# Performance work log

Hardware: AMD Instinct MI355X
Metric: run time of the kernel (lower is better)

Reference implementation:

```python
import jax, jax.numpy as jnp
import numpy as np


def _unpack_int4(w_i32):
    # w_i32: [N, K//8] int32, 8 signed int4 nibbles per int32 (low nibble first)
    shifts = jnp.arange(8, dtype=jnp.int32) * 4
    nib = (w_i32[:, :, None] >> shifts[None, None, :]) & 0xF  # [N, K//8, 8]
    signed = (nib ^ 8) - 8  # map [0,15] -> [-8,7]
    N = w_i32.shape[0]
    return signed.reshape(N, -1)  # [N, K] int32 in [-8,7]


def setup_inputs() -> dict:
    key = jax.random.key(0)
    k1, k2, k3, k4, k5 = jax.random.split(key, 5)
    M, K, N, G = 4096, 4096, 14336, 128
    qx = jax.random.normal(k1, (M, K), dtype=jnp.float32)
    qxscale = jax.random.uniform(k2, (M, 1), dtype=jnp.float32, minval=0.5, maxval=1.5)
    weight_i4 = jax.random.randint(k3, (N, K // 8), 0, 2147483647, dtype=jnp.int32)
    weight_scale = jax.random.uniform(k4, (N, K // G), dtype=jnp.float32, minval=0.001, maxval=0.02)
    bias = jax.random.normal(k5, (N,), dtype=jnp.float32) * 0.02
    return {"qx": qx, "qxscale": qxscale, "weight_i4": weight_i4,
            "weight_scale": weight_scale, "bias": bias, "group_size": G}


def reference(qx, qxscale, weight_i4, weight_scale, bias, group_size):
    # 1) unpack int32 -> int4  2) per-group dequant  3) matmul  4) scale+bias  5) silu
    iweight = _unpack_int4(weight_i4)  # [N, K]
    N, K = iweight.shape
    deq_w = (iweight.astype(jnp.float32).reshape(N, K // group_size, group_size)
             * weight_scale[:, :, None]).reshape(N, K)  # [N, K]
    y = jnp.einsum('mk,nk->mn', qx, deq_w) * qxscale  # [M, N]
    y = y + bias[None, :]
    return jax.nn.silu(y)
```

## Files before the change

kernel.cpp:

```cpp
#include <hip/hip_runtime.h>
#include <hip/hip_bf16.h>
#include <stdint.h>


#define M_DIM 4096
#define K_DIM 4096
#define N_DIM 14336
#define GSZ   128

typedef __bf16 bf16x8 __attribute__((ext_vector_type(8)));
typedef __bf16 bf16x4 __attribute__((ext_vector_type(4)));
typedef float  f32x4  __attribute__((ext_vector_type(4)));

#define GLOAD16(g, l) __builtin_amdgcn_global_load_lds( \
    (const __attribute__((address_space(1))) void*)(g), \
    (__attribute__((address_space(3))) void*)(l), 16, 0, 0)

#define WAITVM(N) asm volatile("s_waitcnt vmcnt(" #N ")" ::: "memory")
#define WAITLGKM0() asm volatile("s_waitcnt lgkmcnt(0)" ::: "memory")


__global__ __launch_bounds__(256) void convertA_kernel(
    const float* __restrict__ qx, __bf16* __restrict__ out)
{
    const size_t i = ((size_t)blockIdx.x * 256 + threadIdx.x) * 8;
    const float4 a = *(const float4*)(qx + i);
    const float4 b = *(const float4*)(qx + i + 4);
    bf16x8 v;
    v[0] = (__bf16)a.x; v[1] = (__bf16)a.y; v[2] = (__bf16)a.z; v[3] = (__bf16)a.w;
    v[4] = (__bf16)b.x; v[5] = (__bf16)b.y; v[6] = (__bf16)b.z; v[7] = (__bf16)b.w;
    *(bf16x8*)(out + i) = v;
}

__global__ __launch_bounds__(256) void dequantW_kernel(
    const int* __restrict__ wq, const float* __restrict__ wscale,
    __bf16* __restrict__ out)
{
    const size_t g = (size_t)blockIdx.x * 256 + threadIdx.x;
    const int n  = (int)(g >> 9);
    const int wi = (int)(g & 511);
    const float s = wscale[(size_t)n * (K_DIM / GSZ) + (wi >> 4)];
    const int w = wq[g];
    bf16x8 v;
    #pragma unroll
    for (int j = 0; j < 8; ++j) {
        const int q = ((int)((unsigned)w << (28 - 4 * j))) >> 28;
        v[j] = (__bf16)((float)q * s);
    }
    *(bf16x8*)(out + g * 8) = v;
}


constexpr int BM = 256, BN = 256, BK = 64;
constexpr int NT  = K_DIM / BK;
constexpr int NIT = NT / 2;
constexpr int BUF_BYTES = 65536;

__global__ __launch_bounds__(512, 2) void gemm256_kernel(
    const __bf16* __restrict__ A,
    const __bf16* __restrict__ B,
    const float* __restrict__ qxscale,
    const float* __restrict__ bias,
    float* __restrict__ out)
{
    __shared__ __align__(16) char smem[2 * BUF_BYTES];

    const int t    = threadIdx.x;
    const int lane = t & 63;
    const int wave = t >> 6;
    const int wr   = wave >> 2;
    const int wc   = wave & 3;

    const int bid = blockIdx.x;
    const int cpx = (M_DIM / BM) * (N_DIM / BN) / 8;
    const int wg  = (bid & 7) * cpx + (bid >> 3);
    const int tiles_n = N_DIM / BN;
    const int tm = wg / tiles_n, tn = wg % tiles_n;
    const int m0 = tm * BM, n0 = tn * BN;

    const int srow = t >> 3;
    const int sg16 = (((t & 7) ^ (srow & 7)) << 4);
    const size_t KB = (size_t)K_DIM * 2;
    const char* aS = (const char*)A + (size_t)(m0 + srow) * KB + sg16;
    const char* bS = (const char*)B + (size_t)(n0 + srow) * KB + sg16;
    char* sbase = smem;

    auto STAGE_AQ = [&](int tile, int q) {
        GLOAD16(aS + (size_t)tile * 128 + (size_t)q * 64 * KB,
                sbase + (tile & 1) * BUF_BYTES + q * 8192 + t * 16);
    };
    auto STAGE_BQ = [&](int tile, int q) {
        GLOAD16(bS + (size_t)tile * 128 + (size_t)q * 64 * KB,
                sbase + (tile & 1) * BUF_BYTES + 32768 + q * 8192 + t * 16);
    };

    const int lane15 = lane & 15;
    const int lc     = lane >> 4;
    const int swzc   = ((lc ^ (lane15 & 7)) << 4);
    const int aR0 = (wr * 128 + lane15) * 128 + swzc;
    const int aR1 = aR0 ^ 64;
    const int bR0 = 32768 + (wc * 64 + lane15) * 128 + swzc;
    const int bR1 = bR0 ^ 64;

    f32x4 acc[8][4] = {};
    bf16x8 af[4][2], bfl[2][2], bfh[2][2];

    auto DS_AF = [&](const char* buf, int mibase) {
        #pragma unroll
        for (int mi = 0; mi < 4; ++mi) {
            af[mi][0] = *(const bf16x8*)(buf + aR0 + (mibase + mi) * 2048);
            af[mi][1] = *(const bf16x8*)(buf + aR1 + (mibase + mi) * 2048);
        }
    };
    auto DS_BL = [&](const char* buf) {
        #pragma unroll
        for (int ni = 0; ni < 2; ++ni) {
            bfl[ni][0] = *(const bf16x8*)(buf + bR0 + ni * 2048);
            bfl[ni][1] = *(const bf16x8*)(buf + bR1 + ni * 2048);
        }
    };
    auto DS_BH = [&](const char* buf) {
        #pragma unroll
        for (int ni = 0; ni < 2; ++ni) {
            bfh[ni][0] = *(const bf16x8*)(buf + bR0 + (2 + ni) * 2048);
            bfh[ni][1] = *(const bf16x8*)(buf + bR1 + (2 + ni) * 2048);
        }
    };
    auto MFMAQ_L = [&](int mo) {
        #pragma unroll
        for (int kk = 0; kk < 2; ++kk)
            #pragma unroll
            for (int mi = 0; mi < 4; ++mi)
                #pragma unroll
                for (int ni = 0; ni < 2; ++ni)
                    acc[mo + mi][ni] = __builtin_amdgcn_mfma_f32_16x16x32_bf16(
                        af[mi][kk], bfl[ni][kk], acc[mo + mi][ni], 0, 0, 0);
    };
    auto MFMAQ_H = [&](int mo) {
        #pragma unroll
        for (int kk = 0; kk < 2; ++kk)
            #pragma unroll
            for (int mi = 0; mi < 4; ++mi)
                #pragma unroll
                for (int ni = 0; ni < 2; ++ni)
                    acc[mo + mi][2 + ni] = __builtin_amdgcn_mfma_f32_16x16x32_bf16(
                        af[mi][kk], bfh[ni][kk], acc[mo + mi][2 + ni], 0, 0, 0);
    };

    #define PH_SYNC() do { __builtin_amdgcn_s_barrier(); WAITLGKM0(); \
        __builtin_amdgcn_sched_barrier(0); __builtin_amdgcn_s_setprio(1); } while (0)
    #define PH_END() do { __builtin_amdgcn_s_setprio(0); \
        __builtin_amdgcn_s_barrier(); } while (0)

    #pragma unroll
    for (int q = 0; q < 4; ++q) STAGE_AQ(0, q);
    #pragma unroll
    for (int q = 0; q < 4; ++q) STAGE_BQ(0, q);
    STAGE_AQ(1, 0); STAGE_AQ(1, 2);
    #pragma unroll
    for (int q = 0; q < 4; ++q) STAGE_BQ(1, q);
    WAITVM(6);
    __builtin_amdgcn_s_barrier();
    __builtin_amdgcn_sched_barrier(0);

    for (int i = 0; i < NIT; ++i) {
        const int t0 = 2 * i, t1 = 2 * i + 1;
        const bool more = (i + 1 < NIT);
        const char* bufE = sbase;
        const char* bufO = sbase + BUF_BYTES;

        DS_AF(bufE, 0); DS_BL(bufE);
        STAGE_AQ(t1, 1); STAGE_AQ(t1, 3);
        PH_SYNC(); MFMAQ_L(0); PH_END();

        DS_BH(bufE);
        if (more) { STAGE_AQ(t0 + 2, 0); STAGE_AQ(t0 + 2, 2); }
        PH_SYNC(); MFMAQ_H(0); PH_END();

        DS_AF(bufE, 4);
        if (more) { STAGE_BQ(t0 + 2, 0); STAGE_BQ(t0 + 2, 1); }
        PH_SYNC(); MFMAQ_H(4); PH_END();

        if (more) { STAGE_BQ(t0 + 2, 2); STAGE_BQ(t0 + 2, 3); WAITVM(6); }
        else      { WAITVM(0); }
        __builtin_amdgcn_s_barrier();
        __builtin_amdgcn_sched_barrier(0);
        __builtin_amdgcn_s_setprio(1);
        MFMAQ_L(4);
        PH_END();

        DS_AF(bufO, 0); DS_BL(bufO);
        if (more) { STAGE_AQ(t0 + 2, 1); STAGE_AQ(t0 + 2, 3); }
        PH_SYNC(); MFMAQ_L(0); PH_END();

        DS_BH(bufO);
        if (more) { STAGE_AQ(t1 + 2, 0); STAGE_AQ(t1 + 2, 2); }
        PH_SYNC(); MFMAQ_H(0); PH_END();

        DS_AF(bufO, 4);
        if (more) { STAGE_BQ(t1 + 2, 0); STAGE_BQ(t1 + 2, 1); }
        PH_SYNC(); MFMAQ_H(4); PH_END();

        if (more) { STAGE_BQ(t1 + 2, 2); STAGE_BQ(t1 + 2, 3); WAITVM(6); }
        __builtin_amdgcn_s_barrier();
        __builtin_amdgcn_sched_barrier(0);
        __builtin_amdgcn_s_setprio(1);
        MFMAQ_L(4);
        PH_END();
    }

    #undef PH_SYNC
    #undef PH_END

    const int c_col = lane & 15;
    const int c_r4  = (lane >> 4) * 4;
    #pragma unroll
    for (int mi = 0; mi < 8; ++mi) {
        const int mg = m0 + wr * 128 + mi * 16 + c_r4;
        float qs[4];
        #pragma unroll
        for (int r = 0; r < 4; ++r) qs[r] = qxscale[mg + r];
        #pragma unroll
        for (int ni = 0; ni < 4; ++ni) {
            const int ng = n0 + wc * 64 + ni * 16 + c_col;
            const float bv = bias[ng];
            #pragma unroll
            for (int r = 0; r < 4; ++r) {
                const float y = acc[mi][ni][r] * qs[r] + bv;
                out[(size_t)(mg + r) * N_DIM + ng] = y / (1.f + __expf(-y));
            }
        }
    }
}


constexpr int FBM = 128, FBN = 128, FBK = 64;
constexpr int FLDA = 72;

__global__ __launch_bounds__(256) void gateproj_fused_kernel(
    const float* __restrict__ qx, const float* __restrict__ qxscale,
    const int* __restrict__ wq, const float* __restrict__ wscale,
    const float* __restrict__ bias, float* __restrict__ out)
{
    __shared__ __bf16 sA[FBM * FLDA];
    __shared__ __bf16 sB[FBN * FLDA];

    const int tid  = threadIdx.x;
    const int lane = tid & 63;
    const int wave = tid >> 6;
    const int wm = wave >> 1, wn = wave & 1;

    const int bid = blockIdx.x;
    const int cpx = (M_DIM / FBM) * (N_DIM / FBN) / 8;
    const int wg  = (bid & 7) * cpx + (bid >> 3);
    const int tiles_n = N_DIM / FBN;
    const int tm = wg / tiles_n, tn = wg % tiles_n;
    const int m0 = tm * FBM, n0 = tn * FBN;

    const int a_row = tid >> 4;
    const int a_col = (tid & 15) * 4;
    const float* aPtr = qx + (size_t)(m0 + a_row) * K_DIM + a_col;

    const int b_row = tid >> 1;
    const int b_wb  = (tid & 1) * 4;
    const int*   bPtr = wq     + (size_t)(n0 + b_row) * (K_DIM / 8) + b_wb;
    const float* sPtr = wscale + (size_t)(n0 + b_row) * (K_DIM / GSZ);

    float4 aReg[8];
    int    bRegW[4];
    float  bScl;
    f32x4 acc[4][4] = {};

    auto LOAD = [&](int kt) {
        const float* ap = aPtr + kt * FBK;
        #pragma unroll
        for (int i = 0; i < 8; ++i)
            aReg[i] = *(const float4*)(ap + (size_t)i * 16 * K_DIM);
        int4 b = *(const int4*)(bPtr + kt * 8);
        bRegW[0] = b.x; bRegW[1] = b.y; bRegW[2] = b.z; bRegW[3] = b.w;
        bScl = sPtr[kt >> 1];
    };

    auto STORE = [&]() {
        #pragma unroll
        for (int i = 0; i < 8; ++i) {
            bf16x4 v;
            v[0] = (__bf16)aReg[i].x; v[1] = (__bf16)aReg[i].y;
            v[2] = (__bf16)aReg[i].z; v[3] = (__bf16)aReg[i].w;
            *(bf16x4*)&sA[(a_row + i * 16) * FLDA + a_col] = v;
        }
        const int cb = (tid & 1) * 32;
        #pragma unroll
        for (int wi = 0; wi < 4; ++wi) {
            const int w = bRegW[wi];
            bf16x8 o;
            #pragma unroll
            for (int j = 0; j < 8; ++j) {
                const int v = ((int)((unsigned)w << (28 - 4 * j))) >> 28;
                o[j] = (__bf16)((float)v * bScl);
            }
            *(bf16x8*)&sB[b_row * FLDA + cb + wi * 8] = o;
        }
    };

    LOAD(0); STORE(); __syncthreads();

    const int FNT = K_DIM / FBK;
    for (int kt = 0; kt < FNT; ++kt) {
        if (kt + 1 < FNT) LOAD(kt + 1);
        #pragma unroll
        for (int kk = 0; kk < 2; ++kk) {
            bf16x8 af[4], bfr[4];
            const int ko = kk * 32 + (lane >> 4) * 8;
            #pragma unroll
            for (int mi = 0; mi < 4; ++mi)
                af[mi] = *(const bf16x8*)&sA[(wm * 64 + mi * 16 + (lane & 15)) * FLDA + ko];
            #pragma unroll
            for (int ni = 0; ni < 4; ++ni)
                bfr[ni] = *(const bf16x8*)&sB[(wn * 64 + ni * 16 + (lane & 15)) * FLDA + ko];
            #pragma unroll
            for (int mi = 0; mi < 4; ++mi)
                #pragma unroll
                for (int ni = 0; ni < 4; ++ni)
                    acc[mi][ni] = __builtin_amdgcn_mfma_f32_16x16x32_bf16(
                        af[mi], bfr[ni], acc[mi][ni], 0, 0, 0);
        }
        __syncthreads();
        if (kt + 1 < FNT) { STORE(); __syncthreads(); }
    }

    const int c_col = lane & 15;
    const int c_r4  = (lane >> 4) * 4;
    #pragma unroll
    for (int mi = 0; mi < 4; ++mi) {
        const int mg = m0 + wm * 64 + mi * 16 + c_r4;
        float qs[4];
        #pragma unroll
        for (int r = 0; r < 4; ++r) qs[r] = qxscale[mg + r];
        #pragma unroll
        for (int ni = 0; ni < 4; ++ni) {
            const int ng = n0 + wn * 64 + ni * 16 + c_col;
            const float bv = bias[ng];
            #pragma unroll
            for (int r = 0; r < 4; ++r) {
                const float y = acc[mi][ni][r] * qs[r] + bv;
                out[(size_t)(mg + r) * N_DIM + ng] = y / (1.f + __expf(-y));
            }
        }
    }
}


extern "C" void kernel_launch(void* const* d_in, const int* in_sizes, int n_in,
                              void* d_out, int out_size, void* d_ws, size_t ws_size,
                              hipStream_t stream) {
    const float* qx      = (const float*)d_in[0];
    const float* qxscale = (const float*)d_in[1];
    const int*   wq      = (const int*)d_in[2];
    const float* wscale  = (const float*)d_in[3];
    const float* bias    = (const float*)d_in[4];
    float* out = (float*)d_out;

    const size_t needA = (size_t)M_DIM * K_DIM * 2;
    const size_t needW = (size_t)N_DIM * K_DIM * 2;

    if (ws_size >= needA + needW) {
        __bf16* Abf = (__bf16*)d_ws;
        __bf16* Wbf = Abf + (size_t)M_DIM * K_DIM;

        hipLaunchKernelGGL(convertA_kernel, dim3(M_DIM * K_DIM / 8 / 256), dim3(256),
                           0, stream, qx, Abf);
        hipLaunchKernelGGL(dequantW_kernel, dim3(N_DIM * (K_DIM / 8) / 256), dim3(256),
                           0, stream, wq, wscale, Wbf);

        const int grid = (M_DIM / BM) * (N_DIM / BN);
        hipLaunchKernelGGL(gemm256_kernel, dim3(grid), dim3(512), 0, stream,
                           Abf, Wbf, qxscale, bias, out);
    } else {
        const int grid = (M_DIM / FBM) * (N_DIM / FBN);
        hipLaunchKernelGGL(gateproj_fused_kernel, dim3(grid), dim3(256), 0, stream,
                           qx, qxscale, wq, wscale, bias, out);
    }
}
```

Baseline: 502.8 us.

## Switch main GEMM from 16x16x32 to 32x32x16 bf16 MFMA tiles

Replaces the 16x16x32 MFMA micro-tiling in the pipelined GEMM with 32x32x16 MFMAs. Each wave now holds a 4x2 grid of 32x32 accumulators, and the LDS fragment reads are reorganised to match, using an XOR swizzle per k-chunk. The epilogue is rewritten for the 32x32 output layout. The goal is fewer LDS fragment reads per FLOP and better MFMA throughput per instruction. The risk is a wrong swizzle or layout mapping and different register pressure.

```diff
diff --git a/kernel.cpp b/kernel.cpp
--- a/kernel.cpp
+++ b/kernel.cpp
@@ -11,6 +11,7 @@
 typedef __bf16 bf16x8 __attribute__((ext_vector_type(8)));
 typedef __bf16 bf16x4 __attribute__((ext_vector_type(4)));
 typedef float  f32x4  __attribute__((ext_vector_type(4)));
+typedef float  f32x16 __attribute__((ext_vector_type(16)));
 
 #define GLOAD16(g, l) __builtin_amdgcn_global_load_lds( \
     (const __attribute__((address_space(1))) void*)(g), \
@@ -94,57 +95,36 @@
                 sbase + (tile & 1) * BUF_BYTES + 32768 + q * 8192 + t * 16);
     };
 
-    const int lane15 = lane & 15;
-    const int lc     = lane >> 4;
-    const int swzc   = ((lc ^ (lane15 & 7)) << 4);
-    const int aR0 = (wr * 128 + lane15) * 128 + swzc;
-    const int aR1 = aR0 ^ 64;
-    const int bR0 = 32768 + (wc * 64 + lane15) * 128 + swzc;
-    const int bR1 = bR0 ^ 64;
-
-    f32x4 acc[8][4] = {};
-    bf16x8 af[4][2], bfl[2][2], bfh[2][2];
-
-    auto DS_AF = [&](const char* buf, int mibase) {
-        #pragma unroll
-        for (int mi = 0; mi < 4; ++mi) {
-            af[mi][0] = *(const bf16x8*)(buf + aR0 + (mibase + mi) * 2048);
-            af[mi][1] = *(const bf16x8*)(buf + aR1 + (mibase + mi) * 2048);
-        }
-    };
-    auto DS_BL = [&](const char* buf) {
-        #pragma unroll
-        for (int ni = 0; ni < 2; ++ni) {
-            bfl[ni][0] = *(const bf16x8*)(buf + bR0 + ni * 2048);
-            bfl[ni][1] = *(const bf16x8*)(buf + bR1 + ni * 2048);
-        }
-    };
-    auto DS_BH = [&](const char* buf) {
-        #pragma unroll
-        for (int ni = 0; ni < 2; ++ni) {
-            bfh[ni][0] = *(const bf16x8*)(buf + bR0 + (2 + ni) * 2048);
-            bfh[ni][1] = *(const bf16x8*)(buf + bR1 + (2 + ni) * 2048);
-        }
-    };
-    auto MFMAQ_L = [&](int mo) {
-        #pragma unroll
-        for (int kk = 0; kk < 2; ++kk)
-            #pragma unroll
-            for (int mi = 0; mi < 4; ++mi)
-                #pragma unroll
-                for (int ni = 0; ni < 2; ++ni)
-                    acc[mo + mi][ni] = __builtin_amdgcn_mfma_f32_16x16x32_bf16(
-                        af[mi][kk], bfl[ni][kk], acc[mo + mi][ni], 0, 0, 0);
-    };
-    auto MFMAQ_H = [&](int mo) {
-        #pragma unroll
-        for (int kk = 0; kk < 2; ++kk)
-            #pragma unroll
-            for (int mi = 0; mi < 4; ++mi)
-                #pragma unroll
-                for (int ni = 0; ni < 2; ++ni)
-                    acc[mo + mi][2 + ni] = __builtin_amdgcn_mfma_f32_16x16x32_bf16(
-                        af[mi][kk], bfh[ni][kk], acc[mo + mi][2 + ni], 0, 0, 0);
+    const int lane31 = lane & 31;
+    const int h      = lane >> 5;
+    const int swz0   = ((h ^ (lane31 & 7)) << 4);
+    const int aB = (wr * 128 + lane31) * 128 + swz0;
+    const int bB = 32768 + (wc * 64 + lane31) * 128 + swz0;
+
+    f32x16 acc[4][2] = {};
+    bf16x8 af[2][4], bfr[2][4];
+
+    auto DS_A = [&](const char* buf, int mibase) {
+        #pragma unroll
+        for (int mi = 0; mi < 2; ++mi)
+            #pragma unroll
+            for (int kk = 0; kk < 4; ++kk)
+                af[mi][kk] = *(const bf16x8*)(buf +
+                    ((aB + (mibase + mi) * 4096) ^ (kk << 5)));
+    };
+    auto DS_B = [&](const char* buf, int ni) {
+        #pragma unroll
+        for (int kk = 0; kk < 4; ++kk)
+            bfr[ni][kk] = *(const bf16x8*)(buf +
+                ((bB + ni * 4096) ^ (kk << 5)));
+    };
+    auto MQ = [&](int mib, int ni) {
+        #pragma unroll
+        for (int kk = 0; kk < 4; ++kk)
+            #pragma unroll
+            for (int mi = 0; mi < 2; ++mi)
+                acc[mib + mi][ni] = __builtin_amdgcn_mfma_f32_32x32x16_bf16(
+                    af[mi][kk], bfr[ni][kk], acc[mib + mi][ni], 0, 0, 0);
     };
 
     #define PH_SYNC() do { __builtin_amdgcn_s_barrier(); WAITLGKM0(); \
@@ -169,65 +149,71 @@
         const char* bufE = sbase;
         const char* bufO = sbase + BUF_BYTES;
 
-        DS_AF(bufE, 0); DS_BL(bufE);
+        DS_A(bufE, 0); DS_B(bufE, 0);
         STAGE_AQ(t1, 1); STAGE_AQ(t1, 3);
-        PH_SYNC(); MFMAQ_L(0); PH_END();
-
-        DS_BH(bufE);
+        PH_SYNC(); MQ(0, 0); PH_END();
+
+        DS_B(bufE, 1);
         if (more) { STAGE_AQ(t0 + 2, 0); STAGE_AQ(t0 + 2, 2); }
-        PH_SYNC(); MFMAQ_H(0); PH_END();
-
-        DS_AF(bufE, 4);
+        PH_SYNC(); MQ(0, 1); PH_END();
+
+        DS_A(bufE, 2);
         if (more) { STAGE_BQ(t0 + 2, 0); STAGE_BQ(t0 + 2, 1); }
-        PH_SYNC(); MFMAQ_H(4); PH_END();
+        PH_SYNC(); MQ(2, 1); PH_END();
 
         if (more) { STAGE_BQ(t0 + 2, 2); STAGE_BQ(t0 + 2, 3); WAITVM(6); }
         else      { WAITVM(0); }
         __builtin_amdgcn_s_barrier();
         __builtin_amdgcn_sched_barrier(0);
         __builtin_amdgcn_s_setprio(1);
-        MFMAQ_L(4);
+        MQ(2, 0);
         PH_END();
 
-        DS_AF(bufO, 0); DS_BL(bufO);
+        DS_A(bufO, 0); DS_B(bufO, 0);
         if (more) { STAGE_AQ(t0 + 2, 1); STAGE_AQ(t0 + 2, 3); }
-        PH_SYNC(); MFMAQ_L(0); PH_END();
-
-        DS_BH(bufO);
+        PH_SYNC(); MQ(0, 0); PH_END();
+
+        DS_B(bufO, 1);
         if (more) { STAGE_AQ(t1 + 2, 0); STAGE_AQ(t1 + 2, 2); }
-        PH_SYNC(); MFMAQ_H(0); PH_END();
-
-        DS_AF(bufO, 4);
+        PH_SYNC(); MQ(0, 1); PH_END();
+
+        DS_A(bufO, 2);
         if (more) { STAGE_BQ(t1 + 2, 0); STAGE_BQ(t1 + 2, 1); }
-        PH_SYNC(); MFMAQ_H(4); PH_END();
+        PH_SYNC(); MQ(2, 1); PH_END();
 
         if (more) { STAGE_BQ(t1 + 2, 2); STAGE_BQ(t1 + 2, 3); WAITVM(6); }
         __builtin_amdgcn_s_barrier();
         __builtin_amdgcn_sched_barrier(0);
         __builtin_amdgcn_s_setprio(1);
-        MFMAQ_L(4);
+        MQ(2, 0);
         PH_END();
     }
 
     #undef PH_SYNC
     #undef PH_END
 
-    const int c_col = lane & 15;
-    const int c_r4  = (lane >> 4) * 4;
-    #pragma unroll
-    for (int mi = 0; mi < 8; ++mi) {
-        const int mg = m0 + wr * 128 + mi * 16 + c_r4;
-        float qs[4];
-        #pragma unroll
-        for (int r = 0; r < 4; ++r) qs[r] = qxscale[mg + r];
-        #pragma unroll
-        for (int ni = 0; ni < 4; ++ni) {
-            const int ng = n0 + wc * 64 + ni * 16 + c_col;
-            const float bv = bias[ng];
-            #pragma unroll
-            for (int r = 0; r < 4; ++r) {
-                const float y = acc[mi][ni][r] * qs[r] + bv;
-                out[(size_t)(mg + r) * N_DIM + ng] = y / (1.f + __expf(-y));
+    const int c_col = lane31;
+    const int hh4   = h * 4;
+    float bv[2];
+    #pragma unroll
+    for (int ni = 0; ni < 2; ++ni)
+        bv[ni] = bias[n0 + wc * 64 + ni * 32 + c_col];
+    #pragma unroll
+    for (int mi = 0; mi < 4; ++mi) {
+        #pragma unroll
+        for (int rq = 0; rq < 4; ++rq) {
+            const int mg = m0 + wr * 128 + mi * 32 + rq * 8 + hh4;
+            float qs[4];
+            #pragma unroll
+            for (int r = 0; r < 4; ++r) qs[r] = qxscale[mg + r];
+            #pragma unroll
+            for (int ni = 0; ni < 2; ++ni) {
+                const int ng = n0 + wc * 64 + ni * 32 + c_col;
+                #pragma unroll
+                for (int r = 0; r < 4; ++r) {
+                    const float y = acc[mi][ni][rq * 4 + r] * qs[r] + bv[ni];
+                    out[(size_t)(mg + r) * N_DIM + ng] = y / (1.f + __expf(-y));
+                }
             }
         }
     }
@@ -310,20 +296,20 @@
         if (kt + 1 < FNT) LOAD(kt + 1);
         #pragma unroll
         for (int kk = 0; kk < 2; ++kk) {
-            bf16x8 af[4], bfr[4];
+            bf16x8 af2[4], bfr2[4];
             const int ko = kk * 32 + (lane >> 4) * 8;
             #pragma unroll
             for (int mi = 0; mi < 4; ++mi)
-                af[mi] = *(const bf16x8*)&sA[(wm * 64 + mi * 16 + (lane & 15)) * FLDA + ko];
+                af2[mi] = *(const bf16x8*)&sA[(wm * 64 + mi * 16 + (lane & 15)) * FLDA + ko];
             #pragma unroll
             for (int ni = 0; ni < 4; ++ni)
-                bfr[ni] = *(const bf16x8*)&sB[(wn * 64 + ni * 16 + (lane & 15)) * FLDA + ko];
+                bfr2[ni] = *(const bf16x8*)&sB[(wn * 64 + ni * 16 + (lane & 15)) * FLDA + ko];
             #pragma unroll
             for (int mi = 0; mi < 4; ++mi)
                 #pragma unroll
                 for (int ni = 0; ni < 4; ++ni)
                     acc[mi][ni] = __builtin_amdgcn_mfma_f32_16x16x32_bf16(
-                        af[mi], bfr[ni], acc[mi][ni], 0, 0, 0);
+                        af2[mi], bfr2[ni], acc[mi][ni], 0, 0, 0);
         }
         __syncthreads();
         if (kt + 1 < FNT) { STORE(); __syncthreads(); }
```

Result: slower. 584.1 us (+16.2%).
